# Optimization experiments

Hardware: AMD Instinct MI355X
Metric: run time of the kernel (lower is better)

Reference implementation:

```python
import jax, jax.numpy as jnp
import numpy as np

N = 50000
E = 800000
IN_DIM = 128
OUT_DIM = 128
EDGE_DIM = 3
H = 4
HD = OUT_DIM // H  # 32
SCALE = HD ** -0.5


def setup_inputs() -> dict:
    key = jax.random.key(0)
    ks = jax.random.split(key, 10)
    x = jax.random.normal(ks[0], (N, IN_DIM), dtype=jnp.float32)
    edge_index = jax.random.randint(ks[1], (2, E), 0, N, dtype=jnp.int64)
    edge_attr = jax.random.normal(ks[2], (E, EDGE_DIM), dtype=jnp.float32)
    s = 1.0 / np.sqrt(IN_DIM)
    Wq = jax.random.normal(ks[3], (IN_DIM, H * HD), dtype=jnp.float32) * s
    Wk = jax.random.normal(ks[4], (IN_DIM, H * HD), dtype=jnp.float32) * s
    Wv = jax.random.normal(ks[5], (IN_DIM, H * HD), dtype=jnp.float32) * s
    We = jax.random.normal(ks[6], (EDGE_DIM, H), dtype=jnp.float32) * (1.0 / np.sqrt(EDGE_DIM))
    Wo = jax.random.normal(ks[7], (H * HD, OUT_DIM), dtype=jnp.float32) * (1.0 / np.sqrt(H * HD))
    bo = jnp.zeros((OUT_DIM,), dtype=jnp.float32)
    Wm = jax.random.normal(ks[8], (IN_DIM + OUT_DIM, OUT_DIM), dtype=jnp.float32) * (1.0 / np.sqrt(IN_DIM + OUT_DIM))
    bm = jnp.zeros((OUT_DIM,), dtype=jnp.float32)
    return {"x": x, "edge_index": edge_index, "edge_attr": edge_attr,
            "Wq": Wq, "Wk": Wk, "Wv": Wv, "We": We, "Wo": Wo, "bo": bo,
            "Wm": Wm, "bm": bm}


def reference(x, edge_index, edge_attr, Wq, Wk, Wv, We, Wo, bo, Wm, bm):
    n = x.shape[0]
    src = edge_index[0]
    dst = edge_index[1]
    Q = (x @ Wq).reshape(n, H, HD)
    K = (x @ Wk).reshape(n, H, HD)
    V = (x @ Wv).reshape(n, H, HD)
    edge_bias = edge_attr @ We                                  # [E, H]
    attn = jnp.sum(Q[dst] * K[src], axis=-1) * SCALE + edge_bias  # [E, H]
    attn = jnp.where(attn >= 0, attn, 0.2 * attn)               # leaky_relu(0.2)
    # NOTE: original uses a single GLOBAL max over all edges/heads for stability
    attn_exp = jnp.exp(attn - jnp.max(attn))
    attn_sum = jax.ops.segment_sum(attn_exp, dst, num_segments=n)  # [N, H]
    attn_norm = attn_exp / jnp.maximum(attn_sum[dst], 1e-12)
    # dropout disabled (eval mode)
    weighted_V = V[src] * attn_norm[:, :, None]                 # [E, H, HD]
    agg = jax.ops.segment_sum(weighted_V, dst, num_segments=n)  # [N, H, HD]
    agg = agg.reshape(n, H * HD) @ Wo + bo                      # [N, OUT]
    h = jnp.concatenate([x, agg], axis=1) @ Wm + bm
    return jax.nn.relu(h)
```

## Files before the change

kernel.cpp:

```cpp
#include <hip/hip_runtime.h>
#include <hip/hip_bf16.h>
#include <math.h>

#define NN 50000
#define NE 800000
#define DIM 128
#define NH 4
#define HD 32
#define EH (NE * NH)
#define ATTN_SCALE 0.17677669529663687f
#define MTILE 64
#define GEMM_BLOCKS 782
#define NBKT 98
#define PTS 2048
#define PBLKS 391
#define HBLKS 104

typedef unsigned int uint;
typedef unsigned short ushort;
typedef __attribute__((ext_vector_type(8))) short short8;
typedef __attribute__((ext_vector_type(4))) float f32x4;

__device__ inline ushort f2bf(float f) {
    __hip_bfloat16 h = __float2bfloat16(f);
    return *(ushort*)&h;
}
__device__ inline float bflo(uint u) { return __uint_as_float(u << 16); }
__device__ inline float bfhi(uint u) { return __uint_as_float(u & 0xffff0000u); }

__global__ __launch_bounds__(256) void prep_x_kernel(
    const float* __restrict__ x, ushort* __restrict__ xb)
{
    const int i = blockIdx.x * 256 + threadIdx.x;
    const float4 v = ((const float4*)x)[i];
    ushort4 o;
    o.x = f2bf(v.x); o.y = f2bf(v.y); o.z = f2bf(v.z); o.w = f2bf(v.w);
    ((ushort4*)xb)[i] = o;
}

__global__ __launch_bounds__(128) void prep_wx_kernel(
    const float* __restrict__ Wo, const float* __restrict__ Wm,
    float* __restrict__ Wx)
{
    const int r = blockIdx.x, j = threadIdx.x;
    float acc = 0.f;
    for (int t = 0; t < 128; ++t)
        acc = fmaf(Wo[r * 128 + t], Wm[(128 + t) * 128 + j], acc);
    Wx[r * 128 + j] = acc;
}

__global__ __launch_bounds__(128) void prep_bias_kernel(
    const float* __restrict__ bo, const float* __restrict__ bm,
    const float* __restrict__ Wm, float* __restrict__ bprime)
{
    const int j = threadIdx.x;
    float acc = bm[j];
    for (int t = 0; t < 128; ++t)
        acc = fmaf(bo[t], Wm[(128 + t) * 128 + j], acc);
    bprime[j] = acc;
}

__global__ __launch_bounds__(256) void pack_qkv_kernel(
    const float* __restrict__ Wq, const float* __restrict__ Wk,
    const float* __restrict__ Wv, short* __restrict__ Bp)
{
    const int idx = blockIdx.x * 256 + threadIdx.x;
    const int j = idx & 7, lane = (idx >> 3) & 63;
    const int rest = idx >> 9;
    const int nt = rest % 24, kc = rest / 24;
    const int k = kc * 32 + (lane >> 4) * 8 + j;
    const int n = nt * 16 + (lane & 15);
    const float* W = (n < 128) ? Wq : (n < 256 ? Wk : Wv);
    Bp[idx] = (short)f2bf(W[k * 128 + (n & 127)]);
}

__global__ __launch_bounds__(256) void pack_out_kernel(
    const float* __restrict__ Wm, const float* __restrict__ Wx,
    short* __restrict__ Bp)
{
    const int idx = blockIdx.x * 256 + threadIdx.x;
    const int j = idx & 7, lane = (idx >> 3) & 63;
    const int rest = idx >> 9;
    const int nt = rest & 7, kc = rest >> 3;
    const int k = kc * 32 + (lane >> 4) * 8 + j;
    const int n = nt * 16 + (lane & 15);
    const float v = (k < 128) ? Wm[k * 128 + n] : Wx[(k - 128) * 128 + n];
    Bp[idx] = (short)f2bf(v);
}

__global__ __launch_bounds__(128) void bkt_zero_kernel(int* __restrict__ bkt_cnt)
{
    if (threadIdx.x < 128) bkt_cnt[threadIdx.x] = 0;
}

__global__ __launch_bounds__(256) void bkt_hist_kernel(
    const int* __restrict__ dst, int* __restrict__ bkt_cnt)
{
    __shared__ int c[NBKT];
    const int tid = threadIdx.x;
    if (tid < NBKT) c[tid] = 0;
    __syncthreads();
    for (int e = blockIdx.x * 256 + tid; e < NE; e += HBLKS * 256)
        atomicAdd(&c[dst[e] >> 9], 1);
    __syncthreads();
    if (tid < NBKT && c[tid]) atomicAdd(&bkt_cnt[tid], c[tid]);
}

__global__ void bkt_scan_kernel(const int* __restrict__ bkt_cnt,
                                int* __restrict__ bkt_base,
                                int* __restrict__ bkt_cursor,
                                int* __restrict__ rowptr)
{
    if (threadIdx.x == 0) {
        int run = 0;
        for (int b = 0; b < NBKT; ++b) {
            bkt_base[b] = run;
            bkt_cursor[b] = run;
            run += bkt_cnt[b];
        }
        bkt_base[NBKT] = run;
        rowptr[NN] = run;
    }
}

__global__ __launch_bounds__(256) void partition_kernel(
    const int* __restrict__ src, const int* __restrict__ dst,
    const float* __restrict__ edge_attr, const float* __restrict__ We,
    int* __restrict__ bkt_cursor,
    int* __restrict__ psrc, int* __restrict__ pdst, float* __restrict__ peb)
{
    __shared__ int cnt[NBKT], rbase[NBKT], cnt2[NBKT];
    const int tid = threadIdx.x;
    if (tid < NBKT) cnt[tid] = 0;
    __syncthreads();
    const int e0 = blockIdx.x * PTS;
    #pragma unroll
    for (int it = 0; it < 8; ++it) {
        const int e = e0 + it * 256 + tid;
        if (e < NE) atomicAdd(&cnt[dst[e] >> 9], 1);
    }
    __syncthreads();
    if (tid < NBKT) {
        rbase[tid] = cnt[tid] ? atomicAdd(&bkt_cursor[tid], cnt[tid]) : 0;
        cnt2[tid] = 0;
    }
    __syncthreads();
    #pragma unroll
    for (int it = 0; it < 8; ++it) {
        const int e = e0 + it * 256 + tid;
        if (e < NE) {
            const int d = dst[e];
            const int b = d >> 9;
            const int r = atomicAdd(&cnt2[b], 1);
            const int pos = rbase[b] + r;
            psrc[pos] = src[e];
            pdst[pos] = d;
            const float a0 = edge_attr[e * 3 + 0];
            const float a1 = edge_attr[e * 3 + 1];
            const float a2 = edge_attr[e * 3 + 2];
            float4 eb;
            eb.x = a0 * We[0] + a1 * We[4] + a2 * We[8];
            eb.y = a0 * We[1] + a1 * We[5] + a2 * We[9];
            eb.z = a0 * We[2] + a1 * We[6] + a2 * We[10];
            eb.w = a0 * We[3] + a1 * We[7] + a2 * We[11];
            *(float4*)(peb + (size_t)pos * 4) = eb;
        }
    }
}

__global__ __launch_bounds__(256) void bucket_csr_kernel(
    const int* __restrict__ bkt_base,
    const int* __restrict__ psrc, const int* __restrict__ pdst,
    const float* __restrict__ peb,
    int* __restrict__ rowptr,
    int* __restrict__ srcp, float* __restrict__ eb_csr)
{
    __shared__ int cnt[512];
    __shared__ int pre[512];
    __shared__ int sc[256];
    const int tid = threadIdx.x;
    const int b = blockIdx.x;
    const int base = bkt_base[b];
    const int n = bkt_base[b + 1] - base;
    const int node0 = b << 9;

    cnt[tid] = 0; cnt[tid + 256] = 0;
    __syncthreads();
    for (int i = base + tid; i < base + n; i += 256)
        atomicAdd(&cnt[pdst[i] - node0], 1);
    __syncthreads();

    const int pair = cnt[2 * tid] + cnt[2 * tid + 1];
    sc[tid] = pair;
    __syncthreads();
    for (int off = 1; off < 256; off <<= 1) {
        const int v = (tid >= off) ? sc[tid - off] : 0;
        __syncthreads();
        sc[tid] += v;
        __syncthreads();
    }
    const int ex = sc[tid] - pair;
    pre[2 * tid] = base + ex;
    pre[2 * tid + 1] = base + ex + cnt[2 * tid];
    __syncthreads();

    for (int l = tid; l < 512; l += 256) {
        const int g = node0 + l;
        if (g < NN) rowptr[g] = pre[l];
    }
    __syncthreads();

    for (int i = base + tid; i < base + n; i += 256) {
        const int d = pdst[i];
        const int pos = atomicAdd(&pre[d - node0], 1);
        srcp[pos] = psrc[i];
        *(float4*)(eb_csr + (size_t)pos * 4) =
            *(const float4*)(peb + (size_t)i * 4);
    }
}

__global__ __launch_bounds__(256) void qkv_mfma_kernel(
    const ushort* __restrict__ xb, const short* __restrict__ Bp,
    ushort* __restrict__ Qb, ushort* __restrict__ Kb, ushort* __restrict__ Vb)
{
    const int wave = threadIdx.x >> 6;
    const int lane = threadIdx.x & 63;
    const int m = lane & 15, quad = lane >> 4;
    const int row0w = blockIdx.x * MTILE + wave * 16;
    const int arow = row0w + m;
    const bool rowok = arow < NN;

    short8 a[4];
    #pragma unroll
    for (int kc = 0; kc < 4; ++kc)
        a[kc] = rowok ? *(const short8*)(xb + (size_t)arow * 128 + kc * 32 + quad * 8)
                      : (short8)(0);

    const int NT = 24;
    for (int nt = 0; nt < NT; nt += 2) {
        f32x4 acc0 = {0.f, 0.f, 0.f, 0.f}, acc1 = {0.f, 0.f, 0.f, 0.f};
        #pragma unroll
        for (int kc = 0; kc < 4; ++kc) {
            const short8 b0 = *(const short8*)(Bp + ((size_t)(kc * NT + nt) * 64 + lane) * 8);
            const short8 b1 = *(const short8*)(Bp + ((size_t)(kc * NT + nt + 1) * 64 + lane) * 8);
            acc0 = __builtin_amdgcn_mfma_f32_16x16x32_bf16(a[kc], b0, acc0, 0, 0, 0);
            acc1 = __builtin_amdgcn_mfma_f32_16x16x32_bf16(a[kc], b1, acc1, 0, 0, 0);
        }
        #pragma unroll
        for (int t = 0; t < 2; ++t) {
            const f32x4 acc = t ? acc1 : acc0;
            const int c = (nt + t) * 16 + m;
            ushort* dstp_ = (c < 128) ? Qb : (c < 256 ? Kb : Vb);
            const int lc = c & 127;
            #pragma unroll
            for (int g = 0; g < 4; ++g) {
                const int r = row0w + quad * 4 + g;
                if (r < NN) dstp_[(size_t)r * 128 + lc] = f2bf(acc[g]);
            }
        }
    }
}

__global__ __launch_bounds__(256) void out_mfma_kernel(
    const ushort* __restrict__ xb, const ushort* __restrict__ aggb,
    const short* __restrict__ Bp, const float* __restrict__ bprime,
    float* __restrict__ out)
{
    const int wave = threadIdx.x >> 6;
    const int lane = threadIdx.x & 63;
    const int m = lane & 15, quad = lane >> 4;
    const int row0w = blockIdx.x * MTILE + wave * 16;
    const int arow = row0w + m;
    const bool rowok = arow < NN;

    short8 a[8];
    #pragma unroll
    for (int kc = 0; kc < 4; ++kc)
        a[kc] = rowok ? *(const short8*)(xb + (size_t)arow * 128 + kc * 32 + quad * 8)
                      : (short8)(0);
    #pragma unroll
    for (int kc = 0; kc < 4; ++kc)
        a[4 + kc] = rowok ? *(const short8*)(aggb + (size_t)arow * 128 + kc * 32 + quad * 8)
                          : (short8)(0);

    const int NT = 8;
    for (int nt = 0; nt < NT; nt += 2) {
        f32x4 acc0 = {0.f, 0.f, 0.f, 0.f}, acc1 = {0.f, 0.f, 0.f, 0.f};
        #pragma unroll
        for (int kc = 0; kc < 8; ++kc) {
            const short8 b0 = *(const short8*)(Bp + ((size_t)(kc * NT + nt) * 64 + lane) * 8);
            const short8 b1 = *(const short8*)(Bp + ((size_t)(kc * NT + nt + 1) * 64 + lane) * 8);
            acc0 = __builtin_amdgcn_mfma_f32_16x16x32_bf16(a[kc], b0, acc0, 0, 0, 0);
            acc1 = __builtin_amdgcn_mfma_f32_16x16x32_bf16(a[kc], b1, acc1, 0, 0, 0);
        }
        #pragma unroll
        for (int t = 0; t < 2; ++t) {
            const f32x4 acc = t ? acc1 : acc0;
            const int c = (nt + t) * 16 + m;
            const float bb = bprime[c];
            #pragma unroll
            for (int g = 0; g < 4; ++g) {
                const int r = row0w + quad * 4 + g;
                if (r < NN) out[(size_t)r * 128 + c] = fmaxf(acc[g] + bb, 0.f);
            }
        }
    }
}

__global__ __launch_bounds__(256) void attn_agg_kernel(
    const ushort* __restrict__ Qb, const ushort* __restrict__ Kb,
    const ushort* __restrict__ Vb,
    const int* __restrict__ rowptr, const int* __restrict__ srcp,
    const float* __restrict__ eb_csr, ushort* __restrict__ aggb)
{
    const int tid = threadIdx.x;
    const int d = blockIdx.x * 4 + (tid >> 6);
    const int lane = tid & 63;
    const int g = lane >> 4;
    const int t = lane & 15;
    const int h = t >> 2;
    const int begin = rowptr[d];
    const int end   = rowptr[d + 1];

    const uint4 uq = *(const uint4*)(Qb + (size_t)d * DIM + 8 * t);
    float q0 = bflo(uq.x), q1 = bfhi(uq.x);
    float q2 = bflo(uq.y), q3 = bfhi(uq.y);
    float q4 = bflo(uq.z), q5 = bfhi(uq.z);
    float q6 = bflo(uq.w), q7 = bfhi(uq.w);

    float ss = 0.f;
    float a0 = 0.f, a1 = 0.f, a2 = 0.f, a3 = 0.f;
    float a4 = 0.f, a5 = 0.f, a6 = 0.f, a7 = 0.f;

    if (begin < end) {
        int ec = begin + g;
        if (ec >= end) ec = end - 1;
        int s   = srcp[ec];
        float eb = eb_csr[(size_t)ec * 4 + h];

        for (int p = begin; p < end; p += 4) {
            const bool ok = (p + g) < end;
            const int pn = p + 4;
            int sn = s; float ebn = eb;
            if (pn < end) {
                int en = pn + g;
                if (en >= end) en = end - 1;
                sn  = srcp[en];
                ebn = eb_csr[(size_t)en * 4 + h];
            }

            const uint4 uk = *(const uint4*)(Kb + (size_t)s * DIM + 8 * t);
            const uint4 uv = *(const uint4*)(Vb + (size_t)s * DIM + 8 * t);

            float da = q0 * bflo(uk.x);
            float db = q1 * bfhi(uk.x);
            da = fmaf(q2, bflo(uk.y), da);
            db = fmaf(q3, bfhi(uk.y), db);
            da = fmaf(q4, bflo(uk.z), da);
            db = fmaf(q5, bfhi(uk.z), db);
            da = fmaf(q6, bflo(uk.w), da);
            db = fmaf(q7, bfhi(uk.w), db);
            float part = da + db;
            part += __shfl_xor(part, 1);
            part += __shfl_xor(part, 2);

            float a = fmaf(part, ATTN_SCALE, eb);
            a = (a >= 0.f) ? a : 0.2f * a;
            float w = ok ? __expf(a) : 0.f;

            ss += w;
            a0 = fmaf(w, bflo(uv.x), a0);
            a1 = fmaf(w, bfhi(uv.x), a1);
            a2 = fmaf(w, bflo(uv.y), a2);
            a3 = fmaf(w, bfhi(uv.y), a3);
            a4 = fmaf(w, bflo(uv.z), a4);
            a5 = fmaf(w, bfhi(uv.z), a5);
            a6 = fmaf(w, bflo(uv.w), a6);
            a7 = fmaf(w, bfhi(uv.w), a7);

            s = sn; eb = ebn;
        }
    }

    ss += __shfl_xor(ss, 16);
    ss += __shfl_xor(ss, 32);
    a0 += __shfl_xor(a0, 16); a0 += __shfl_xor(a0, 32);
    a1 += __shfl_xor(a1, 16); a1 += __shfl_xor(a1, 32);
    a2 += __shfl_xor(a2, 16); a2 += __shfl_xor(a2, 32);
    a3 += __shfl_xor(a3, 16); a3 += __shfl_xor(a3, 32);
    a4 += __shfl_xor(a4, 16); a4 += __shfl_xor(a4, 32);
    a5 += __shfl_xor(a5, 16); a5 += __shfl_xor(a5, 32);
    a6 += __shfl_xor(a6, 16); a6 += __shfl_xor(a6, 32);
    a7 += __shfl_xor(a7, 16); a7 += __shfl_xor(a7, 32);

    if (g == 0) {
        const float inv = 1.f / fmaxf(ss, 1e-12f);
        uint4 o;
        o.x = (uint)f2bf(a0 * inv) | ((uint)f2bf(a1 * inv) << 16);
        o.y = (uint)f2bf(a2 * inv) | ((uint)f2bf(a3 * inv) << 16);
        o.z = (uint)f2bf(a4 * inv) | ((uint)f2bf(a5 * inv) << 16);
        o.w = (uint)f2bf(a6 * inv) | ((uint)f2bf(a7 * inv) << 16);
        *(uint4*)(aggb + (size_t)d * DIM + 8 * t) = o;
    }
}

extern "C" void kernel_launch(void* const* d_in, const int* in_sizes, int n_in,
                              void* d_out, int out_size, void* d_ws, size_t ws_size,
                              hipStream_t stream)
{
    const float* x         = (const float*)d_in[0];
    const int*   edge_idx  = (const int*)d_in[1];
    const float* edge_attr = (const float*)d_in[2];
    const float* Wq        = (const float*)d_in[3];
    const float* Wk        = (const float*)d_in[4];
    const float* Wv        = (const float*)d_in[5];
    const float* We        = (const float*)d_in[6];
    const float* Wo        = (const float*)d_in[7];
    const float* bo        = (const float*)d_in[8];
    const float* Wm        = (const float*)d_in[9];
    const float* bm        = (const float*)d_in[10];
    float* out = (float*)d_out;

    const int* src = edge_idx;
    const int* dst = edge_idx + NE;

    ushort* xb   = (ushort*)d_ws;
    ushort* Qb   = xb + (size_t)NN * DIM;
    ushort* Kb   = Qb + (size_t)NN * DIM;
    ushort* Vb   = Kb + (size_t)NN * DIM;
    ushort* aggb = Vb + (size_t)NN * DIM;
    int*   psrc     = (int*)(aggb + (size_t)NN * DIM);
    int*   pdst     = psrc + NE;
    float* peb      = (float*)(pdst + NE);
    float* eb_csr   = peb + (size_t)EH;
    float* Wx       = eb_csr + (size_t)EH;
    float* bprime   = Wx + 16384;
    short* BpQKV    = (short*)(bprime + 128);
    short* BpOut    = BpQKV + 49152;
    int*   rowptr   = (int*)(BpOut + 32768);
    int*   srcp     = rowptr + 50048;
    int*   bkt_cnt    = srcp + NE;
    int*   bkt_base   = bkt_cnt + 128;
    int*   bkt_cursor = bkt_base + 128;

    prep_x_kernel<<<(NN * DIM / 4) / 256, 256, 0, stream>>>(x, xb);
    prep_wx_kernel<<<128, 128, 0, stream>>>(Wo, Wm, Wx);
    prep_bias_kernel<<<1, 128, 0, stream>>>(bo, bm, Wm, bprime);
    pack_qkv_kernel<<<192, 256, 0, stream>>>(Wq, Wk, Wv, BpQKV);
    pack_out_kernel<<<128, 256, 0, stream>>>(Wm, Wx, BpOut);

    bkt_zero_kernel<<<1, 128, 0, stream>>>(bkt_cnt);
    bkt_hist_kernel<<<HBLKS, 256, 0, stream>>>(dst, bkt_cnt);
    bkt_scan_kernel<<<1, 64, 0, stream>>>(bkt_cnt, bkt_base, bkt_cursor, rowptr);
    partition_kernel<<<PBLKS, 256, 0, stream>>>(src, dst, edge_attr, We,
                                                bkt_cursor, psrc, pdst, peb);
    bucket_csr_kernel<<<NBKT, 256, 0, stream>>>(bkt_base, psrc, pdst, peb,
                                                rowptr, srcp, eb_csr);

    qkv_mfma_kernel<<<GEMM_BLOCKS, 256, 0, stream>>>(xb, BpQKV, Qb, Kb, Vb);
    attn_agg_kernel<<<NN / 4, 256, 0, stream>>>(Qb, Kb, Vb, rowptr, srcp,
                                                eb_csr, aggb);
    out_mfma_kernel<<<GEMM_BLOCKS, 256, 0, stream>>>(xb, aggb, BpOut, bprime, out);
}
```

Baseline: 287.5 us.

## Merge prep and partition/QKV kernels via block-range dispatch, compress edge data

Folds the weight packing, Wx/bias precompute, histogram and x-to-bf16 conversion into one launch that picks its task by block index. It also runs the edge partition, the QKV MFMA GEMM and the output weight packing together in a second merged launch. Edge records are packed: src and local dst share one 32-bit word, edge bias is stored as bf16, and the CSR source index is 16-bit. This is meant to cut launch count and memory traffic in the CSR build and attention gather. The cost is lower edge-bias precision, and 16-bit source indices only hold because N=50000 fits in 16 bits.

```diff
diff --git a/kernel.cpp b/kernel.cpp
--- a/kernel.cpp
+++ b/kernel.cpp
@@ -7,14 +7,22 @@
 #define DIM 128
 #define NH 4
 #define HD 32
-#define EH (NE * NH)
 #define ATTN_SCALE 0.17677669529663687f
 #define MTILE 64
 #define GEMM_BLOCKS 782
 #define NBKT 98
 #define PTS 2048
-#define PBLKS 391
 #define HBLKS 104
+
+#define PREP_QKV_BASE  104
+#define PREP_WXB_BASE  296
+#define PREP_X_BASE    361
+#define PREP_GRID      6611
+
+#define PQ_PART_N   391
+#define PQ_QKV_BASE 391
+#define PQ_PACKO_BASE 1173
+#define PQ_GRID     1301
 
 typedef unsigned int uint;
 typedef unsigned short ushort;
@@ -27,83 +35,58 @@
 }
 __device__ inline float bflo(uint u) { return __uint_as_float(u << 16); }
 __device__ inline float bfhi(uint u) { return __uint_as_float(u & 0xffff0000u); }
-
-__global__ __launch_bounds__(256) void prep_x_kernel(
-    const float* __restrict__ x, ushort* __restrict__ xb)
-{
-    const int i = blockIdx.x * 256 + threadIdx.x;
-    const float4 v = ((const float4*)x)[i];
-    ushort4 o;
-    o.x = f2bf(v.x); o.y = f2bf(v.y); o.z = f2bf(v.z); o.w = f2bf(v.w);
-    ((ushort4*)xb)[i] = o;
-}
-
-__global__ __launch_bounds__(128) void prep_wx_kernel(
+__device__ inline float bf2f(ushort u) { return __uint_as_float((uint)u << 16); }
+
+__global__ __launch_bounds__(256) void prep_all_kernel(
+    const float* __restrict__ x, ushort* __restrict__ xb,
+    const int* __restrict__ dst, int* __restrict__ bkt_cnt,
+    const float* __restrict__ Wq, const float* __restrict__ Wk,
+    const float* __restrict__ Wv, short* __restrict__ BpQKV,
     const float* __restrict__ Wo, const float* __restrict__ Wm,
-    float* __restrict__ Wx)
-{
-    const int r = blockIdx.x, j = threadIdx.x;
-    float acc = 0.f;
-    for (int t = 0; t < 128; ++t)
-        acc = fmaf(Wo[r * 128 + t], Wm[(128 + t) * 128 + j], acc);
-    Wx[r * 128 + j] = acc;
-}
-
-__global__ __launch_bounds__(128) void prep_bias_kernel(
     const float* __restrict__ bo, const float* __restrict__ bm,
-    const float* __restrict__ Wm, float* __restrict__ bprime)
-{
-    const int j = threadIdx.x;
-    float acc = bm[j];
-    for (int t = 0; t < 128; ++t)
-        acc = fmaf(bo[t], Wm[(128 + t) * 128 + j], acc);
-    bprime[j] = acc;
-}
-
-__global__ __launch_bounds__(256) void pack_qkv_kernel(
-    const float* __restrict__ Wq, const float* __restrict__ Wk,
-    const float* __restrict__ Wv, short* __restrict__ Bp)
-{
-    const int idx = blockIdx.x * 256 + threadIdx.x;
-    const int j = idx & 7, lane = (idx >> 3) & 63;
-    const int rest = idx >> 9;
-    const int nt = rest % 24, kc = rest / 24;
-    const int k = kc * 32 + (lane >> 4) * 8 + j;
-    const int n = nt * 16 + (lane & 15);
-    const float* W = (n < 128) ? Wq : (n < 256 ? Wk : Wv);
-    Bp[idx] = (short)f2bf(W[k * 128 + (n & 127)]);
-}
-
-__global__ __launch_bounds__(256) void pack_out_kernel(
-    const float* __restrict__ Wm, const float* __restrict__ Wx,
-    short* __restrict__ Bp)
-{
-    const int idx = blockIdx.x * 256 + threadIdx.x;
-    const int j = idx & 7, lane = (idx >> 3) & 63;
-    const int rest = idx >> 9;
-    const int nt = rest & 7, kc = rest >> 3;
-    const int k = kc * 32 + (lane >> 4) * 8 + j;
-    const int n = nt * 16 + (lane & 15);
-    const float v = (k < 128) ? Wm[k * 128 + n] : Wx[(k - 128) * 128 + n];
-    Bp[idx] = (short)f2bf(v);
-}
-
-__global__ __launch_bounds__(128) void bkt_zero_kernel(int* __restrict__ bkt_cnt)
-{
-    if (threadIdx.x < 128) bkt_cnt[threadIdx.x] = 0;
-}
-
-__global__ __launch_bounds__(256) void bkt_hist_kernel(
-    const int* __restrict__ dst, int* __restrict__ bkt_cnt)
-{
-    __shared__ int c[NBKT];
+    float* __restrict__ Wx, float* __restrict__ bprime)
+{
+    const int bid = blockIdx.x;
     const int tid = threadIdx.x;
-    if (tid < NBKT) c[tid] = 0;
-    __syncthreads();
-    for (int e = blockIdx.x * 256 + tid; e < NE; e += HBLKS * 256)
-        atomicAdd(&c[dst[e] >> 9], 1);
-    __syncthreads();
-    if (tid < NBKT && c[tid]) atomicAdd(&bkt_cnt[tid], c[tid]);
+
+    if (bid < PREP_QKV_BASE) {
+        __shared__ int c[NBKT];
+        if (tid < NBKT) c[tid] = 0;
+        __syncthreads();
+        for (int e = bid * 256 + tid; e < NE; e += HBLKS * 256)
+            atomicAdd(&c[dst[e] >> 9], 1);
+        __syncthreads();
+        if (tid < NBKT && c[tid]) atomicAdd(&bkt_cnt[tid], c[tid]);
+    } else if (bid < PREP_WXB_BASE) {
+        const int idx = (bid - PREP_QKV_BASE) * 256 + tid;
+        const int j = idx & 7, lane = (idx >> 3) & 63;
+        const int rest = idx >> 9;
+        const int nt = rest % 24, kc = rest / 24;
+        const int k = kc * 32 + (lane >> 4) * 8 + j;
+        const int n = nt * 16 + (lane & 15);
+        const float* W = (n < 128) ? Wq : (n < 256 ? Wk : Wv);
+        BpQKV[idx] = (short)f2bf(W[k * 128 + (n & 127)]);
+    } else if (bid < PREP_X_BASE) {
+        const int r = (bid - PREP_WXB_BASE) * 2 + (tid >> 7);
+        const int j = tid & 127;
+        if (r < 128) {
+            float acc = 0.f;
+            for (int t = 0; t < 128; ++t)
+                acc = fmaf(Wo[r * 128 + t], Wm[(128 + t) * 128 + j], acc);
+            Wx[r * 128 + j] = acc;
+        } else if (r == 128) {
+            float acc = bm[j];
+            for (int t = 0; t < 128; ++t)
+                acc = fmaf(bo[t], Wm[(128 + t) * 128 + j], acc);
+            bprime[j] = acc;
+        }
+    } else {
+        const int i = (bid - PREP_X_BASE) * 256 + tid;
+        const float4 v = ((const float4*)x)[i];
+        ushort4 o;
+        o.x = f2bf(v.x); o.y = f2bf(v.y); o.z = f2bf(v.z); o.w = f2bf(v.w);
+        ((ushort4*)xb)[i] = o;
+    }
 }
 
 __global__ void bkt_scan_kernel(const int* __restrict__ bkt_cnt,
@@ -123,57 +106,112 @@
     }
 }
 
-__global__ __launch_bounds__(256) void partition_kernel(
+__global__ __launch_bounds__(256) void partqkv_kernel(
     const int* __restrict__ src, const int* __restrict__ dst,
     const float* __restrict__ edge_attr, const float* __restrict__ We,
     int* __restrict__ bkt_cursor,
-    int* __restrict__ psrc, int* __restrict__ pdst, float* __restrict__ peb)
-{
-    __shared__ int cnt[NBKT], rbase[NBKT], cnt2[NBKT];
+    uint* __restrict__ ppack, uint2* __restrict__ pebp,
+    const ushort* __restrict__ xb, const short* __restrict__ BpQKV,
+    ushort* __restrict__ Qb, ushort* __restrict__ Kb, ushort* __restrict__ Vb,
+    const float* __restrict__ Wm, const float* __restrict__ Wx,
+    short* __restrict__ BpOut)
+{
+    const int bid = blockIdx.x;
     const int tid = threadIdx.x;
-    if (tid < NBKT) cnt[tid] = 0;
-    __syncthreads();
-    const int e0 = blockIdx.x * PTS;
-    #pragma unroll
-    for (int it = 0; it < 8; ++it) {
-        const int e = e0 + it * 256 + tid;
-        if (e < NE) atomicAdd(&cnt[dst[e] >> 9], 1);
-    }
-    __syncthreads();
-    if (tid < NBKT) {
-        rbase[tid] = cnt[tid] ? atomicAdd(&bkt_cursor[tid], cnt[tid]) : 0;
-        cnt2[tid] = 0;
-    }
-    __syncthreads();
-    #pragma unroll
-    for (int it = 0; it < 8; ++it) {
-        const int e = e0 + it * 256 + tid;
-        if (e < NE) {
-            const int d = dst[e];
-            const int b = d >> 9;
-            const int r = atomicAdd(&cnt2[b], 1);
-            const int pos = rbase[b] + r;
-            psrc[pos] = src[e];
-            pdst[pos] = d;
-            const float a0 = edge_attr[e * 3 + 0];
-            const float a1 = edge_attr[e * 3 + 1];
-            const float a2 = edge_attr[e * 3 + 2];
-            float4 eb;
-            eb.x = a0 * We[0] + a1 * We[4] + a2 * We[8];
-            eb.y = a0 * We[1] + a1 * We[5] + a2 * We[9];
-            eb.z = a0 * We[2] + a1 * We[6] + a2 * We[10];
-            eb.w = a0 * We[3] + a1 * We[7] + a2 * We[11];
-            *(float4*)(peb + (size_t)pos * 4) = eb;
-        }
+
+    if (bid < PQ_PART_N) {
+        __shared__ int cnt[NBKT], rbase[NBKT], cnt2[NBKT];
+        if (tid < NBKT) cnt[tid] = 0;
+        __syncthreads();
+        const int e0 = bid * PTS;
+        #pragma unroll
+        for (int it = 0; it < 8; ++it) {
+            const int e = e0 + it * 256 + tid;
+            if (e < NE) atomicAdd(&cnt[dst[e] >> 9], 1);
+        }
+        __syncthreads();
+        if (tid < NBKT) {
+            rbase[tid] = cnt[tid] ? atomicAdd(&bkt_cursor[tid], cnt[tid]) : 0;
+            cnt2[tid] = 0;
+        }
+        __syncthreads();
+        #pragma unroll
+        for (int it = 0; it < 8; ++it) {
+            const int e = e0 + it * 256 + tid;
+            if (e < NE) {
+                const int d = dst[e];
+                const int b = d >> 9;
+                const int r = atomicAdd(&cnt2[b], 1);
+                const int pos = rbase[b] + r;
+                ppack[pos] = (uint)src[e] | ((uint)(d & 511) << 16);
+                const float a0 = edge_attr[e * 3 + 0];
+                const float a1 = edge_attr[e * 3 + 1];
+                const float a2 = edge_attr[e * 3 + 2];
+                const float b0 = a0 * We[0] + a1 * We[4] + a2 * We[8];
+                const float b1 = a0 * We[1] + a1 * We[5] + a2 * We[9];
+                const float b2 = a0 * We[2] + a1 * We[6] + a2 * We[10];
+                const float b3 = a0 * We[3] + a1 * We[7] + a2 * We[11];
+                uint2 ep;
+                ep.x = (uint)f2bf(b0) | ((uint)f2bf(b1) << 16);
+                ep.y = (uint)f2bf(b2) | ((uint)f2bf(b3) << 16);
+                pebp[pos] = ep;
+            }
+        }
+    } else if (bid < PQ_PACKO_BASE) {
+        const int qb = bid - PQ_QKV_BASE;
+        const int wave = tid >> 6;
+        const int lane = tid & 63;
+        const int m = lane & 15, quad = lane >> 4;
+        const int row0w = qb * MTILE + wave * 16;
+        const int arow = row0w + m;
+        const bool rowok = arow < NN;
+
+        short8 a[4];
+        #pragma unroll
+        for (int kc = 0; kc < 4; ++kc)
+            a[kc] = rowok ? *(const short8*)(xb + (size_t)arow * 128 + kc * 32 + quad * 8)
+                          : (short8)(0);
+
+        const int NT = 24;
+        for (int nt = 0; nt < NT; nt += 2) {
+            f32x4 acc0 = {0.f, 0.f, 0.f, 0.f}, acc1 = {0.f, 0.f, 0.f, 0.f};
+            #pragma unroll
+            for (int kc = 0; kc < 4; ++kc) {
+                const short8 b0 = *(const short8*)(BpQKV + ((size_t)(kc * NT + nt) * 64 + lane) * 8);
+                const short8 b1 = *(const short8*)(BpQKV + ((size_t)(kc * NT + nt + 1) * 64 + lane) * 8);
+                acc0 = __builtin_amdgcn_mfma_f32_16x16x32_bf16(a[kc], b0, acc0, 0, 0, 0);
+                acc1 = __builtin_amdgcn_mfma_f32_16x16x32_bf16(a[kc], b1, acc1, 0, 0, 0);
+            }
+            #pragma unroll
+            for (int t = 0; t < 2; ++t) {
+                const f32x4 acc = t ? acc1 : acc0;
+                const int c = (nt + t) * 16 + m;
+                ushort* dstp_ = (c < 128) ? Qb : (c < 256 ? Kb : Vb);
+                const int lc = c & 127;
+                #pragma unroll
+                for (int g = 0; g < 4; ++g) {
+                    const int r = row0w + quad * 4 + g;
+                    if (r < NN) dstp_[(size_t)r * 128 + lc] = f2bf(acc[g]);
+                }
+            }
+        }
+    } else {
+        const int idx = (bid - PQ_PACKO_BASE) * 256 + tid;
+        const int j = idx & 7, lane = (idx >> 3) & 63;
+        const int rest = idx >> 9;
+        const int nt = rest & 7, kc = rest >> 3;
+        const int k = kc * 32 + (lane >> 4) * 8 + j;
+        const int n = nt * 16 + (lane & 15);
+        const float v = (k < 128) ? Wm[k * 128 + n] : Wx[(k - 128) * 128 + n];
+        BpOut[idx] = (short)f2bf(v);
     }
 }
 
 __global__ __launch_bounds__(256) void bucket_csr_kernel(
     const int* __restrict__ bkt_base,
-    const int* __restrict__ psrc, const int* __restrict__ pdst,
-    const float* __restrict__ peb,
+    const uint* __restrict__ ppack, const uint2* __restrict__ pebp,
     int* __restrict__ rowptr,
-    int* __restrict__ srcp, float* __restrict__ eb_csr)
+    ushort* __restrict__ srcp, uint2* __restrict__ ebq)
 {
     __shared__ int cnt[512];
     __shared__ int pre[512];
@@ -187,7 +225,7 @@
     cnt[tid] = 0; cnt[tid + 256] = 0;
     __syncthreads();
     for (int i = base + tid; i < base + n; i += 256)
-        atomicAdd(&cnt[pdst[i] - node0], 1);
+        atomicAdd(&cnt[ppack[i] >> 16], 1);
     __syncthreads();
 
     const int pair = cnt[2 * tid] + cnt[2 * tid + 1];
@@ -211,53 +249,10 @@
     __syncthreads();
 
     for (int i = base + tid; i < base + n; i += 256) {
-        const int d = pdst[i];
-        const int pos = atomicAdd(&pre[d - node0], 1);
-        srcp[pos] = psrc[i];
-        *(float4*)(eb_csr + (size_t)pos * 4) =
-            *(const float4*)(peb + (size_t)i * 4);
-    }
-}
-
-__global__ __launch_bounds__(256) void qkv_mfma_kernel(
-    const ushort* __restrict__ xb, const short* __restrict__ Bp,
-    ushort* __restrict__ Qb, ushort* __restrict__ Kb, ushort* __restrict__ Vb)
-{
-    const int wave = threadIdx.x >> 6;
-    const int lane = threadIdx.x & 63;
-    const int m = lane & 15, quad = lane >> 4;
-    const int row0w = blockIdx.x * MTILE + wave * 16;
-    const int arow = row0w + m;
-    const bool rowok = arow < NN;
-
-    short8 a[4];
-    #pragma unroll
-    for (int kc = 0; kc < 4; ++kc)
-        a[kc] = rowok ? *(const short8*)(xb + (size_t)arow * 128 + kc * 32 + quad * 8)
-                      : (short8)(0);
-
-    const int NT = 24;
-    for (int nt = 0; nt < NT; nt += 2) {
-        f32x4 acc0 = {0.f, 0.f, 0.f, 0.f}, acc1 = {0.f, 0.f, 0.f, 0.f};
-        #pragma unroll
-        for (int kc = 0; kc < 4; ++kc) {
-            const short8 b0 = *(const short8*)(Bp + ((size_t)(kc * NT + nt) * 64 + lane) * 8);
-            const short8 b1 = *(const short8*)(Bp + ((size_t)(kc * NT + nt + 1) * 64 + lane) * 8);
-            acc0 = __builtin_amdgcn_mfma_f32_16x16x32_bf16(a[kc], b0, acc0, 0, 0, 0);
-            acc1 = __builtin_amdgcn_mfma_f32_16x16x32_bf16(a[kc], b1, acc1, 0, 0, 0);
-        }
-        #pragma unroll
-        for (int t = 0; t < 2; ++t) {
-            const f32x4 acc = t ? acc1 : acc0;
-            const int c = (nt + t) * 16 + m;
-            ushort* dstp_ = (c < 128) ? Qb : (c < 256 ? Kb : Vb);
-            const int lc = c & 127;
-            #pragma unroll
-            for (int g = 0; g < 4; ++g) {
-                const int r = row0w + quad * 4 + g;
-                if (r < NN) dstp_[(size_t)r * 128 + lc] = f2bf(acc[g]);
-            }
-        }
+        const uint v = ppack[i];
+        const int pos = atomicAdd(&pre[v >> 16], 1);
+        srcp[pos] = (ushort)(v & 0xFFFFu);
+        ebq[pos] = pebp[i];
     }
 }
 
@@ -310,8 +305,8 @@
 __global__ __launch_bounds__(256) void attn_agg_kernel(
     const ushort* __restrict__ Qb, const ushort* __restrict__ Kb,
     const ushort* __restrict__ Vb,
-    const int* __restrict__ rowptr, const int* __restrict__ srcp,
-    const float* __restrict__ eb_csr, ushort* __restrict__ aggb)
+    const int* __restrict__ rowptr, const ushort* __restrict__ srcp,
+    const ushort* __restrict__ ebb, ushort* __restrict__ aggb)
 {
     const int tid = threadIdx.x;
     const int d = blockIdx.x * 4 + (tid >> 6);
@@ -323,10 +318,10 @@
     const int end   = rowptr[d + 1];
 
     const uint4 uq = *(const uint4*)(Qb + (size_t)d * DIM + 8 * t);
-    float q0 = bflo(uq.x), q1 = bfhi(uq.x);
-    float q2 = bflo(uq.y), q3 = bfhi(uq.y);
-    float q4 = bflo(uq.z), q5 = bfhi(uq.z);
-    float q6 = bflo(uq.w), q7 = bfhi(uq.w);
+    const float q0 = bflo(uq.x), q1 = bfhi(uq.x);
+    const float q2 = bflo(uq.y), q3 = bfhi(uq.y);
+    const float q4 = bflo(uq.z), q5 = bfhi(uq.z);
+    const float q6 = bflo(uq.w), q7 = bfhi(uq.w);
 
     float ss = 0.f;
     float a0 = 0.f, a1 = 0.f, a2 = 0.f, a3 = 0.f;
@@ -335,8 +330,8 @@
     if (begin < end) {
         int ec = begin + g;
         if (ec >= end) ec = end - 1;
-        int s   = srcp[ec];
-        float eb = eb_csr[(size_t)ec * 4 + h];
+        int s    = (int)srcp[ec];
+        float eb = bf2f(ebb[ec * 4 + h]);
 
         for (int p = begin; p < end; p += 4) {
             const bool ok = (p + g) < end;
@@ -345,8 +340,8 @@
             if (pn < end) {
                 int en = pn + g;
                 if (en >= end) en = end - 1;
-                sn  = srcp[en];
-                ebn = eb_csr[(size_t)en * 4 + h];
+                sn  = (int)srcp[en];
+                ebn = bf2f(ebb[en * 4 + h]);
             }
 
             const uint4 uk = *(const uint4*)(Kb + (size_t)s * DIM + 8 * t);
@@ -429,36 +424,35 @@
     ushort* Kb   = Qb + (size_t)NN * DIM;
     ushort* Vb   = Kb + (size_t)NN * DIM;
     ushort* aggb = Vb + (size_t)NN * DIM;
-    int*   psrc     = (int*)(aggb + (size_t)NN * DIM);
-    int*   pdst     = psrc + NE;
-    float* peb      = (float*)(pdst + NE);
-    float* eb_csr   = peb + (size_t)EH;
-    float* Wx       = eb_csr + (size_t)EH;
-    float* bprime   = Wx + 16384;
-    short* BpQKV    = (short*)(bprime + 128);
-    short* BpOut    = BpQKV + 49152;
-    int*   rowptr   = (int*)(BpOut + 32768);
-    int*   srcp     = rowptr + 50048;
-    int*   bkt_cnt    = srcp + NE;
+    uint*  ppack = (uint*)(aggb + (size_t)NN * DIM);
+    uint2* pebp  = (uint2*)(ppack + NE);
+    uint2* ebq   = pebp + NE;
+    ushort* srcp = (ushort*)(ebq + NE);
+    float* Wx    = (float*)(srcp + NE);
+    float* bprime= Wx + 16384;
+    short* BpQKV = (short*)(bprime + 128);
+    short* BpOut = BpQKV + 49152;
+    int*   rowptr= (int*)(BpOut + 32768);
+    int*   bkt_cnt    = rowptr + 50048;
     int*   bkt_base   = bkt_cnt + 128;
     int*   bkt_cursor = bkt_base + 128;
 
-    prep_x_kernel<<<(NN * DIM / 4) / 256, 256, 0, stream>>>(x, xb);
-    prep_wx_kernel<<<128, 128, 0, stream>>>(Wo, Wm, Wx);
-    prep_bias_kernel<<<1, 128, 0, stream>>>(bo, bm, Wm, bprime);
-    pack_qkv_kernel<<<192, 256, 0, stream>>>(Wq, Wk, Wv, BpQKV);
-    pack_out_kernel<<<128, 256, 0, stream>>>(Wm, Wx, BpOut);
-
-    bkt_zero_kernel<<<1, 128, 0, stream>>>(bkt_cnt);
-    bkt_hist_kernel<<<HBLKS, 256, 0, stream>>>(dst, bkt_cnt);
+    hipMemsetAsync(bkt_cnt, 0, 128 * sizeof(int), stream);
+
+    prep_all_kernel<<<PREP_GRID, 256, 0, stream>>>(
+        x, xb, dst, bkt_cnt, Wq, Wk, Wv, BpQKV, Wo, Wm, bo, bm, Wx, bprime);
+
     bkt_scan_kernel<<<1, 64, 0, stream>>>(bkt_cnt, bkt_base, bkt_cursor, rowptr);
-    partition_kernel<<<PBLKS, 256, 0, stream>>>(src, dst, edge_attr, We,
-                                                bkt_cursor, psrc, pdst, peb);
-    bucket_csr_kernel<<<NBKT, 256, 0, stream>>>(bkt_base, psrc, pdst, peb,
-                                                rowptr, srcp, eb_csr);
-
-    qkv_mfma_kernel<<<GEMM_BLOCKS, 256, 0, stream>>>(xb, BpQKV, Qb, Kb, Vb);
+
+    partqkv_kernel<<<PQ_GRID, 256, 0, stream>>>(
+        src, dst, edge_attr, We, bkt_cursor, ppack, pebp,
+        xb, BpQKV, Qb, Kb, Vb, Wm, Wx, BpOut);
+
+    bucket_csr_kernel<<<NBKT, 256, 0, stream>>>(bkt_base, ppack, pebp,
+                                                rowptr, srcp, ebq);
+
     attn_agg_kernel<<<NN / 4, 256, 0, stream>>>(Qb, Kb, Vb, rowptr, srcp,
-                                                eb_csr, aggb);
+                                                (const ushort*)ebq, aggb);
+
     out_mfma_kernel<<<GEMM_BLOCKS, 256, 0, stream>>>(xb, aggb, BpOut, bprime, out);
 }
```

After: 254.1 us. -11.6%, faster.
